# Kernel optimization log

Measured on AMD Instinct MI355X. Metric: run time of the kernel, lower is better.

## Reference

```python
import jax, jax.numpy as jnp
import numpy as np

WS = (7, 7)   # window size
SS = (3, 3)   # shift size
NH = 3        # num heads
EPS = 1e-5


def _rel_index():
    # relative position index [N, N], computed exactly as in WindowAttention.__init__
    coords = np.stack(np.meshgrid(np.arange(WS[0]), np.arange(WS[1]), indexing='ij'))  # [2,7,7]
    cf = coords.reshape(2, -1)                     # [2, N]
    rel = (cf[:, :, None] - cf[:, None, :]).transpose(1, 2, 0)  # [N, N, 2]
    rel[..., 0] += WS[0] - 1
    rel[..., 1] += WS[1] - 1
    idx = rel[..., 0] * (2 * WS[1] - 1) + rel[..., 1]
    return jnp.asarray(idx)


def _attn_mask(H, W):
    # standard Swin shifted-window mask: [nW, N, N] of {0, -100}
    img = np.zeros((H, W), dtype=np.float32)
    cnt = 0
    for hs in (slice(0, -WS[0]), slice(-WS[0], -SS[0]), slice(-SS[0], None)):
        for ws_ in (slice(0, -WS[1]), slice(-WS[1], -SS[1]), slice(-SS[1], None)):
            img[hs, ws_] = cnt
            cnt += 1
    mw = img.reshape(H // WS[0], WS[0], W // WS[1], WS[1]).transpose(0, 2, 1, 3)
    mw = mw.reshape(-1, WS[0] * WS[1])            # [nW, N]
    am = mw[:, None, :] - mw[:, :, None]
    am = np.where(am != 0, np.float32(-100.0), np.float32(0.0))
    return jnp.asarray(am)


def _ln(x, g, b):
    m = x.mean(-1, keepdims=True)
    v = ((x - m) ** 2).mean(-1, keepdims=True)
    return (x - m) * jax.lax.rsqrt(v + EPS) * g + b


def _forward(x, norm1_g, norm1_b, qkv_w, qkv_b, rel_table, proj_w, proj_b,
             norm2_g, norm2_b, mlp_w1, mlp_b1, mlp_w2, mlp_b2):
    B, C, H, W = x.shape
    N = WS[0] * WS[1]
    hd = C // NH
    scale = hd ** -0.5

    # norm1 over channels (token layout [B, HW, C])
    xt = x.reshape(B, C, H * W).transpose(0, 2, 1)
    xn = _ln(xt, norm1_g, norm1_b).transpose(0, 2, 1).reshape(B, C, H, W)

    # cyclic shift + window partition -> [B*nW, N, C]
    shifted = jnp.roll(xn, (-SS[0], -SS[1]), axis=(2, 3))
    nWh, nWw = H // WS[0], W // WS[1]
    xw = shifted.transpose(0, 2, 3, 1)  # [B, H, W, C]
    xwin = xw.reshape(B, nWh, WS[0], nWw, WS[1], C).transpose(0, 1, 3, 2, 4, 5)
    xwin = xwin.reshape(-1, N, C)

    # windowed attention with relative position bias + shift mask
    qkv = (xwin @ qkv_w.T + qkv_b).reshape(-1, N, 3, NH, hd).transpose(2, 0, 3, 1, 4)
    q, k, v = qkv[0] * scale, qkv[1], qkv[2]            # [B_, h, N, hd]
    attn = jnp.einsum('bhnd,bhmd->bhnm', q, k)          # [B_, h, N, N]
    bias = rel_table[_rel_index()]                       # [N, N, h]
    attn = attn + bias.transpose(2, 0, 1)[None]
    mask = _attn_mask(H, W)                              # [nW, N, N]
    nW = mask.shape[0]
    attn = attn.reshape(-1, nW, NH, N, N) + mask[None, :, None]
    attn = jax.nn.softmax(attn.reshape(-1, NH, N, N), axis=-1)
    out = jnp.einsum('bhnm,bhmd->bhnd', attn, v).transpose(0, 2, 1, 3).reshape(-1, N, C)
    out = out @ proj_w.T + proj_b

    # window reverse + reverse shift -> [B, C, H, W]
    xr = out.reshape(B, nWh, nWw, WS[0], WS[1], C).transpose(0, 1, 3, 2, 4, 5)
    xr = xr.reshape(B, H, W, C).transpose(0, 3, 1, 2)
    xr = jnp.roll(xr, (SS[0], SS[1]), axis=(2, 3))

    x = x + xr  # residual (drop_path = Identity)

    # MLP branch with pre-norm over channels
    xt = x.reshape(B, C, H * W).transpose(0, 2, 1)
    h = _ln(xt, norm2_g, norm2_b)
    h = jax.nn.gelu(h @ mlp_w1.T + mlp_b1, approximate=False)
    h = h @ mlp_w2.T + mlp_b2
    return x + h.transpose(0, 2, 1).reshape(B, C, H, W)


def setup_inputs() -> dict:
    key = jax.random.key(0)
    ks = jax.random.split(key, 8)
    B, C, H, W = 8, 96, 224, 224
    hid = 384
    s = 0.02
    return {
        'x': jax.random.normal(ks[0], (B, C, H, W), jnp.float32),
        'norm1_g': jnp.ones((C,), jnp.float32),
        'norm1_b': jnp.zeros((C,), jnp.float32),
        'qkv_w': jax.random.normal(ks[1], (3 * C, C), jnp.float32) * s,
        'qkv_b': jnp.zeros((3 * C,), jnp.float32),
        'rel_table': jax.random.normal(ks[2], (169, NH), jnp.float32) * s,
        'proj_w': jax.random.normal(ks[3], (C, C), jnp.float32) * s,
        'proj_b': jnp.zeros((C,), jnp.float32),
        'norm2_g': jnp.ones((C,), jnp.float32),
        'norm2_b': jnp.zeros((C,), jnp.float32),
        'mlp_w1': jax.random.normal(ks[4], (hid, C), jnp.float32) * s,
        'mlp_b1': jnp.zeros((hid,), jnp.float32),
        'mlp_w2': jax.random.normal(ks[5], (C, hid), jnp.float32) * s,
        'mlp_b2': jnp.zeros((C,), jnp.float32),
    }


def reference(x, norm1_g, norm1_b, qkv_w, qkv_b, rel_table, proj_w, proj_b,
              norm2_g, norm2_b, mlp_w1, mlp_b1, mlp_w2, mlp_b2):
    return _forward(x, norm1_g, norm1_b, qkv_w, qkv_b, rel_table, proj_w, proj_b,
                    norm2_g, norm2_b, mlp_w1, mlp_b1, mlp_w2, mlp_b2)
```

## Files before the change

kernel.cpp:

```cpp
#include <hip/hip_runtime.h>
#include <hip/hip_bf16.h>

typedef __attribute__((ext_vector_type(8))) short short8;
typedef __attribute__((ext_vector_type(4))) short s16x4;
typedef __attribute__((ext_vector_type(4))) float f32x4;

#define D_H   224
#define D_W   224
#define D_HW  50176
#define SCALE 0.17677669529663687f

#define WO_QKVW  0
#define WO_PROJW 27648
#define WO_W1    36864
#define WO_W2    73728
#define WO_TOT   110592

#define XT_SH 0
#define YT_SH 38535168
#define W_SH  77070336
#define WS_NEED ((size_t)(77070336 + 110592) * 2)

static __device__ __forceinline__ short f2s(float v) {
    union { __hip_bfloat16 b; short s; } u; u.b = __float2bfloat16(v); return u.s;
}
static __device__ __forceinline__ float s2f(short s) {
    union { short s; __hip_bfloat16 b; } u; u.s = s; return __bfloat162float(u.b);
}

#define MFMA(a, b, c) __builtin_amdgcn_mfma_f32_16x16x32_bf16((a), (b), (c), 0, 0, 0)

static __device__ __forceinline__ short8 normfrag(const short* p, const float* g,
                                                  const float* b, int c0, float m, float rs) {
    short8 r = *(const short8*)p;
    short8 o;
#pragma unroll
    for (int j = 0; j < 8; j++) o[j] = f2s((s2f(r[j]) - m) * rs * g[c0 + j] + b[c0 + j]);
    return o;
}

static __device__ __forceinline__ float erf_fast(float x) {
    float a = fabsf(x);
    float t = __builtin_amdgcn_rcpf(1.f + 0.3275911f * a);
    float p = t * (0.254829592f + t * (-0.284496736f + t * (1.421413741f +
              t * (-1.453152027f + t * 1.061405429f))));
    float y = 1.f - p * __expf(-a * a);
    return copysignf(y, x);
}

__global__ __launch_bounds__(256) void k_prep(
    const float* __restrict__ qkvw, const float* __restrict__ projw,
    const float* __restrict__ w1, const float* __restrict__ w2, short* __restrict__ ws)
{
    int i4 = blockIdx.x * 256 + threadIdx.x;
    const float* src; int off;
    if (i4 < 6912)        { src = qkvw;  off = 0; }
    else if (i4 < 9216)   { src = projw; off = 6912; }
    else if (i4 < 18432)  { src = w1;    off = 9216; }
    else                  { src = w2;    off = 18432; }
    f32x4 v = *(const f32x4*)&src[(i4 - off) * 4];
    s16x4 s;
#pragma unroll
    for (int j = 0; j < 4; j++) s[j] = f2s(v[j]);
    *(s16x4*)&ws[i4 * 4] = s;
}

__global__ __launch_bounds__(256) void k_t(const float* __restrict__ x, short* __restrict__ xt)
{
    __shared__ short tile[224][96];
    const int tid = threadIdx.x;
    const int bh = blockIdx.x;
    const int b = bh / 224, h = bh - b * 224;
    const int pbase = (b * 96) * D_HW + h * 224;

#pragma unroll
    for (int k = 0; k < 21; k++) {
        int idx = tid + k * 256;
        int w = idx % 224, u = idx / 224;
        int c0 = u * 4;
        s16x4 v;
        v[0] = f2s(x[pbase + (c0 + 0) * D_HW + w]);
        v[1] = f2s(x[pbase + (c0 + 1) * D_HW + w]);
        v[2] = f2s(x[pbase + (c0 + 2) * D_HW + w]);
        v[3] = f2s(x[pbase + (c0 + 3) * D_HW + w]);
        int slot = (u + w) % 24;
        *(s16x4*)&tile[w][slot * 4] = v;
    }
    __syncthreads();
    const int obase = ((b * 224 + h) * 224) * 96;
#pragma unroll
    for (int k = 0; k < 11; k++) {
        int idx = tid + k * 256;
        if (idx < 2688) {
            int w = idx / 12, s = idx - w * 12;
            int sl0 = (s * 2 + w) % 24, sl1 = (s * 2 + 1 + w) % 24;
            s16x4 a = *(const s16x4*)&tile[w][sl0 * 4];
            s16x4 c = *(const s16x4*)&tile[w][sl1 * 4];
            short8 o;
            o[0] = a[0]; o[1] = a[1]; o[2] = a[2]; o[3] = a[3];
            o[4] = c[0]; o[5] = c[1]; o[6] = c[2]; o[7] = c[3];
            *(short8*)&xt[obase + w * 96 + s * 8] = o;
        }
    }
}

__global__ __launch_bounds__(256, 3) void k_attn_t(
    const short* __restrict__ xt, const float* __restrict__ n1g, const float* __restrict__ n1b,
    const float* __restrict__ qkvb, const float* __restrict__ relt,
    const float* __restrict__ projb, const short* __restrict__ wsw, short* __restrict__ yt)
{
    __shared__ short qk[64][200];
    __shared__ __align__(16) short region[11520];
    short (*xs)[104] = (short(*)[104])region;
    short (*ps)[72]  = (short(*)[72])region;
    short (*vt)[72]  = (short(*)[72])(region + 4608);
    __shared__ int   cnt_s[64];
    __shared__ float mean_s[64], rstd_s[64];

    const int tid  = threadIdx.x;
    const int wave = tid >> 6, lane = tid & 63;
    const int l16  = lane & 15, q8 = (lane >> 4) * 8, q4 = (lane >> 4) * 4;
    const int t0   = wave * 16;

    const short* qkvw_bf  = wsw + WO_QKVW;
    const short* projw_bf = wsw + WO_PROJW;

    const int wi = blockIdx.x;
    const int b  = wi >> 10, nw = wi & 1023;
    const int wh = nw >> 5, ww = nw & 31;
    const bool edge = (wh == 31) || (ww == 31);

    if (tid < 64) {
        int t = (tid < 49) ? tid : 48;
        int r = t / 7, c = t - r * 7;
        int sh = wh * 7 + r, sw = ww * 7 + c;
        int rh = (sh < 217) ? 0 : ((sh < 221) ? 1 : 2);
        int rw = (sw < 217) ? 0 : ((sw < 221) ? 1 : 2);
        cnt_s[tid] = rh * 3 + rw;
    }
#pragma unroll
    for (int k = 0; k < 3; k++) {
        int idx = tid + k * 256;
        int t = idx / 12, s = idx - t * 12;
        short8 v = {0, 0, 0, 0, 0, 0, 0, 0};
        if (t < 49) {
            int r = t / 7, cc = t - r * 7;
            int hh = wh * 7 + r + 3;  if (hh >= D_H) hh -= D_H;
            int w2 = ww * 7 + cc + 3; if (w2 >= D_W) w2 -= D_W;
            v = *(const short8*)&xt[((b * 224 + hh) * 224 + w2) * 96 + s * 8];
        }
        *(short8*)&xs[t][s * 8] = v;
    }
    __syncthreads();

    {
        int t = tid >> 2, p = tid & 3;
        float s = 0.f, s2 = 0.f;
#pragma unroll
        for (int i = 0; i < 6; i++) {
            s16x4 v4 = *(const s16x4*)&xs[t][p * 24 + i * 4];
#pragma unroll
            for (int j = 0; j < 4; j++) { float v = s2f(v4[j]); s += v; s2 += v * v; }
        }
        s += __shfl_xor(s, 1); s2 += __shfl_xor(s2, 1);
        s += __shfl_xor(s, 2); s2 += __shfl_xor(s2, 2);
        if (p == 0) {
            float m = s * (1.f / 96.f);
            float var = s2 * (1.f / 96.f) - m * m;
            mean_s[t] = m; rstd_s[t] = rsqrtf(var + 1e-5f);
        }
    }

    const float m0 = mean_s[t0 + l16], rs0 = rstd_s[t0 + l16];
    short8 a0 = normfrag(&xs[t0 + l16][q8],      n1g, n1b, q8,      m0, rs0);
    short8 a1 = normfrag(&xs[t0 + l16][32 + q8], n1g, n1b, 32 + q8, m0, rs0);
    short8 a2 = normfrag(&xs[t0 + l16][64 + q8], n1g, n1b, 64 + q8, m0, rs0);

    short8 wA0, wA1, wA2, wB0, wB1, wB2;
    {
        const short* w = qkvw_bf + l16 * 96;
        wA0 = *(const short8*)&w[q8];
        wA1 = *(const short8*)&w[32 + q8];
        wA2 = *(const short8*)&w[64 + q8];
    }
    __syncthreads();

#pragma unroll
    for (int g = 0; g < 18; g++) {
        const int jc = g / 6, nt = g - jc * 6;
        const int jj = nt * 16 + l16;
        if (g < 17) {
            int g2 = g + 1, jc2 = g2 / 6, nt2 = g2 - jc2 * 6;
            const short* w = qkvw_bf + (jc2 * 96 + nt2 * 16 + l16) * 96;
            wB0 = *(const short8*)&w[q8];
            wB1 = *(const short8*)&w[32 + q8];
            wB2 = *(const short8*)&w[64 + q8];
        }
        f32x4 acc = {0.f, 0.f, 0.f, 0.f};
        acc = MFMA(a0, wA0, acc);
        acc = MFMA(a1, wA1, acc);
        acc = MFMA(a2, wA2, acc);
        float bias = qkvb[jc * 96 + jj];
        if (jc == 0) {
#pragma unroll
            for (int r = 0; r < 4; r++) qk[t0 + q4 + r][jj] = f2s((acc[r] + bias) * SCALE);
        } else if (jc == 1) {
#pragma unroll
            for (int r = 0; r < 4; r++) qk[t0 + q4 + r][96 + jj] = f2s(acc[r] + bias);
        } else {
            s16x4 v4;
#pragma unroll
            for (int r = 0; r < 4; r++) v4[r] = f2s(acc[r] + bias);
            *(s16x4*)&vt[jj][t0 + q4] = v4;
        }
        wA0 = wB0; wA1 = wB1; wA2 = wB2;
    }

    float biasv[4][4][3];
#pragma unroll
    for (int nt = 0; nt < 4; nt++) {
        int m  = nt * 16 + l16;
        int mm = (m < 49) ? m : 48;
        int r2 = mm / 7, c2 = mm - r2 * 7;
        int cm = cnt_s[m];
#pragma unroll
        for (int r = 0; r < 4; r++) {
            int n  = t0 + q4 + r;
            int nn = (n < 49) ? n : 48;
            int r1 = nn / 7, c1 = nn - r1 * 7;
            int ri = ((r1 - r2 + 6) * 13 + (c1 - c2 + 6)) * 3;
            float mk = (edge && (cnt_s[n] != cm)) ? -100.f : 0.f;
            biasv[nt][r][0] = relt[ri + 0] + mk;
            biasv[nt][r][1] = relt[ri + 1] + mk;
            biasv[nt][r][2] = relt[ri + 2] + mk;
        }
    }
    const bool inval3 = (l16 != 0);

    __syncthreads();

#pragma unroll
    for (int h = 0; h < 3; h++) {
        short8 aq = *(const short8*)&qk[t0 + l16][h * 32 + q8];
        f32x4 sv[4];
#pragma unroll
        for (int nt = 0; nt < 4; nt++) {
            f32x4 z = {0.f, 0.f, 0.f, 0.f};
            sv[nt] = MFMA(aq, *(const short8*)&qk[nt * 16 + l16][96 + h * 32 + q8], z);
        }
        float mx[4] = {-1e30f, -1e30f, -1e30f, -1e30f};
#pragma unroll
        for (int nt = 0; nt < 4; nt++) {
#pragma unroll
            for (int r = 0; r < 4; r++) {
                float v = sv[nt][r] + biasv[nt][r][h];
                if (nt == 3 && inval3) v = -1e30f;
                sv[nt][r] = v;
                mx[r] = fmaxf(mx[r], v);
            }
        }
#pragma unroll
        for (int d = 1; d < 16; d <<= 1) {
#pragma unroll
            for (int r = 0; r < 4; r++) mx[r] = fmaxf(mx[r], __shfl_xor(mx[r], d));
        }
        float sm[4] = {0.f, 0.f, 0.f, 0.f};
#pragma unroll
        for (int nt = 0; nt < 4; nt++) {
#pragma unroll
            for (int r = 0; r < 4; r++) {
                float e = (nt == 3 && inval3) ? 0.f : __expf(sv[nt][r] - mx[r]);
                sv[nt][r] = e;
                sm[r] += e;
            }
        }
#pragma unroll
        for (int d = 1; d < 16; d <<= 1) {
#pragma unroll
            for (int r = 0; r < 4; r++) sm[r] += __shfl_xor(sm[r], d);
        }
        float inv[4];
#pragma unroll
        for (int r = 0; r < 4; r++) inv[r] = __builtin_amdgcn_rcpf(sm[r]);
#pragma unroll
        for (int nt = 0; nt < 4; nt++) {
#pragma unroll
            for (int r = 0; r < 4; r++)
                ps[t0 + q4 + r][nt * 16 + l16] = f2s(sv[nt][r] * inv[r]);
        }
        short8 p0 = *(const short8*)&ps[t0 + l16][q8];
        short8 p1 = *(const short8*)&ps[t0 + l16][32 + q8];
#pragma unroll
        for (int nt = 0; nt < 2; nt++) {
            f32x4 acc = {0.f, 0.f, 0.f, 0.f};
            acc = MFMA(p0, *(const short8*)&vt[h * 32 + nt * 16 + l16][q8],      acc);
            acc = MFMA(p1, *(const short8*)&vt[h * 32 + nt * 16 + l16][32 + q8], acc);
            int d = nt * 16 + l16;
#pragma unroll
            for (int r = 0; r < 4; r++) {
                int t = t0 + q4 + r;
                if (t < 49) qk[t][h * 32 + d] = f2s(acc[r]);
            }
        }
    }

    {
        const short* w = projw_bf + l16 * 96;
        wA0 = *(const short8*)&w[q8];
        wA1 = *(const short8*)&w[32 + q8];
        wA2 = *(const short8*)&w[64 + q8];
    }
    short8 o0 = *(const short8*)&qk[t0 + l16][q8];
    short8 o1 = *(const short8*)&qk[t0 + l16][32 + q8];
    short8 o2 = *(const short8*)&qk[t0 + l16][64 + q8];
#pragma unroll
    for (int nt = 0; nt < 6; nt++) {
        int i = nt * 16 + l16;
        if (nt < 5) {
            const short* w = projw_bf + ((nt + 1) * 16 + l16) * 96;
            wB0 = *(const short8*)&w[q8];
            wB1 = *(const short8*)&w[32 + q8];
            wB2 = *(const short8*)&w[64 + q8];
        }
        f32x4 acc = {0.f, 0.f, 0.f, 0.f};
        acc = MFMA(o0, wA0, acc);
        acc = MFMA(o1, wA1, acc);
        acc = MFMA(o2, wA2, acc);
        float pb = projb[i];
#pragma unroll
        for (int r = 0; r < 4; r++) {
            int t = t0 + q4 + r;
            if (t < 49) qk[t][i] = f2s(acc[r] + pb);
        }
        wA0 = wB0; wA1 = wB1; wA2 = wB2;
    }
    __syncthreads();
#pragma unroll
    for (int k = 0; k < 3; k++) {
        int idx = tid + k * 256;
        if (idx < 588) {
            int t = idx / 12, s = idx - t * 12;
            int r = t / 7, cc = t - r * 7;
            int hh = wh * 7 + r + 3;  if (hh >= D_H) hh -= D_H;
            int w2 = ww * 7 + cc + 3; if (w2 >= D_W) w2 -= D_W;
            *(short8*)&yt[((b * 224 + hh) * 224 + w2) * 96 + s * 8] =
                *(const short8*)&qk[t][s * 8];
        }
    }
}

#define XCOL(row, c) ((((((c) >> 3) ^ (((row) >> 2) & 7)) << 3)) | ((c) & 7))

__global__ __launch_bounds__(256, 3) void k_mlp_t(
    const float* __restrict__ x, const short* __restrict__ ytk, float* __restrict__ y,
    const float* __restrict__ n2g, const float* __restrict__ n2b,
    const float* __restrict__ b1, const float* __restrict__ b2, const short* __restrict__ wsw)
{
    __shared__ __align__(16) short xs[64][128];
    __shared__ __align__(16) short wb[96][104];
    __shared__ __align__(16) short hb[64][104];
    __shared__ float mean_s[64], rstd_s[64];

    const int tid  = threadIdx.x;
    const int wave = tid >> 6, lane = tid & 63;
    const int l16  = lane & 15, q8 = (lane >> 4) * 8, q4 = (lane >> 4) * 4;
    const int t0   = wave * 16;

    const short* w1_bf = wsw + WO_W1;
    const short* w2_bf = wsw + WO_W2;

    const int T0 = blockIdx.x * 64;
    const int b  = T0 / D_HW;
    const int p0 = T0 - b * D_HW;
    const int base = (b * 96) * D_HW + p0;

#pragma unroll
    for (int k = 0; k < 3; k++) {
        int idx = tid + k * 256;
        int t = idx / 12, s = idx - t * 12;
        *(short8*)&xs[t][(s ^ ((t >> 2) & 7)) << 3] =
            *(const short8*)&ytk[(T0 + t) * 96 + s * 8];
    }
    __syncthreads();

    float yv[6][4];
#pragma unroll
    for (int k = 0; k < 6; k++) {
        int idx = tid + k * 256;
        int c = idx >> 4, q = idx & 15;
        f32x4 xv = *(const f32x4*)&x[base + c * D_HW + q * 4];
        int ch = ((c >> 3) ^ (q & 7)) * 8 + (c & 7);
#pragma unroll
        for (int j = 0; j < 4; j++) {
            float v = xv[j] + s2f(xs[q * 4 + j][ch]);
            yv[k][j] = v;
            xs[q * 4 + j][ch] = f2s(v);
        }
    }
    __syncthreads();

    {
        int t = tid >> 2, p = tid & 3;
        float s = 0.f, s2 = 0.f;
#pragma unroll
        for (int i = 0; i < 6; i++) {
            int c = p * 24 + i * 4;
            s16x4 v4 = *(const s16x4*)&xs[t][XCOL(t, c)];
#pragma unroll
            for (int j = 0; j < 4; j++) { float v = s2f(v4[j]); s += v; s2 += v * v; }
        }
        s += __shfl_xor(s, 1); s2 += __shfl_xor(s2, 1);
        s += __shfl_xor(s, 2); s2 += __shfl_xor(s2, 2);
        if (p == 0) {
            float m = s * (1.f / 96.f);
            float var = s2 * (1.f / 96.f) - m * m;
            mean_s[t] = m; rstd_s[t] = rsqrtf(var + 1e-5f);
        }
    }

    short8 xa[3];
    {
        int t = t0 + l16;
        float m = mean_s[t], rs = rstd_s[t];
        int key = (t >> 2) & 7;
#pragma unroll
        for (int kk = 0; kk < 3; kk++) {
            int ch = kk * 4 + (lane >> 4);
            xa[kk] = normfrag(&xs[t][(ch ^ key) << 3], n2g, n2b, ch * 8, m, rs);
        }
    }

    f32x4 c2[6];
#pragma unroll
    for (int nt = 0; nt < 6; nt++) c2[nt] = (f32x4){0.f, 0.f, 0.f, 0.f};

    short8 pf[5];
#pragma unroll
    for (int k = 0; k < 5; k++) {
        int idx = tid + k * 256; if (idx > 1151) idx = 1151;
        pf[k] = *(const short8*)&w1_bf[idx * 8];
    }
#pragma unroll
    for (int jc = 0; jc < 4; jc++) {
        if (jc > 0) __syncthreads();
#pragma unroll
        for (int k = 0; k < 5; k++) {
            int idx = tid + k * 256;
            if (idx < 1152) { int j = idx / 12, s = idx - j * 12; *(short8*)&wb[j][s * 8] = pf[k]; }
        }
        __syncthreads();
#pragma unroll
        for (int k = 0; k < 5; k++) {
            int idx = tid + k * 256; if (idx > 1151) idx = 1151;
            int o = idx / 12, s = idx - o * 12;
            pf[k] = *(const short8*)&w2_bf[o * 384 + jc * 96 + s * 8];
        }
#pragma unroll
        for (int nt = 0; nt < 6; nt++) {
            int jj = nt * 16 + l16;
            f32x4 acc = {0.f, 0.f, 0.f, 0.f};
            acc = MFMA(xa[0], *(const short8*)&wb[jj][q8],      acc);
            acc = MFMA(xa[1], *(const short8*)&wb[jj][32 + q8], acc);
            acc = MFMA(xa[2], *(const short8*)&wb[jj][64 + q8], acc);
            float bb = b1[jc * 96 + jj];
#pragma unroll
            for (int r = 0; r < 4; r++) {
                float v = acc[r] + bb;
                float g = 0.5f * v * (1.f + erf_fast(v * 0.7071067811865475f));
                hb[t0 + q4 + r][jj] = f2s(g);
            }
        }
        __syncthreads();
#pragma unroll
        for (int k = 0; k < 5; k++) {
            int idx = tid + k * 256;
            if (idx < 1152) { int j = idx / 12, s = idx - j * 12; *(short8*)&wb[j][s * 8] = pf[k]; }
        }
        __syncthreads();
        if (jc < 3) {
#pragma unroll
            for (int k = 0; k < 5; k++) {
                int idx = tid + k * 256; if (idx > 1151) idx = 1151;
                pf[k] = *(const short8*)&w1_bf[(jc + 1) * 9216 + idx * 8];
            }
        }
        {
            short8 h0 = *(const short8*)&hb[t0 + l16][q8];
            short8 h1 = *(const short8*)&hb[t0 + l16][32 + q8];
            short8 h2 = *(const short8*)&hb[t0 + l16][64 + q8];
#pragma unroll
            for (int nt = 0; nt < 6; nt++) {
                int jj = nt * 16 + l16;
                c2[nt] = MFMA(h0, *(const short8*)&wb[jj][q8],      c2[nt]);
                c2[nt] = MFMA(h1, *(const short8*)&wb[jj][32 + q8], c2[nt]);
                c2[nt] = MFMA(h2, *(const short8*)&wb[jj][64 + q8], c2[nt]);
            }
        }
    }

#pragma unroll
    for (int nt = 0; nt < 6; nt++) {
        int i = nt * 16 + l16;
        float bo = b2[i];
#pragma unroll
        for (int r = 0; r < 4; r++) {
            int t = t0 + q4 + r;
            xs[t][XCOL(t, i)] = f2s(bo + c2[nt][r]);
        }
    }
    __syncthreads();
#pragma unroll
    for (int k = 0; k < 6; k++) {
        int idx = tid + k * 256;
        int c = idx >> 4, q = idx & 15;
        int ch = ((c >> 3) ^ (q & 7)) * 8 + (c & 7);
        f32x4 o;
#pragma unroll
        for (int j = 0; j < 4; j++) o[j] = yv[k][j] + s2f(xs[q * 4 + j][ch]);
        *(f32x4*)&y[base + c * D_HW + q * 4] = o;
    }
}

__global__ __launch_bounds__(256, 3) void k_attn_f(
    const float* __restrict__ x, const float* __restrict__ n1g, const float* __restrict__ n1b,
    const float* __restrict__ qkvb, const float* __restrict__ relt,
    const float* __restrict__ projb, const short* __restrict__ wsw, float* __restrict__ y)
{
    __shared__ short qk[64][200];
    __shared__ short vt[96][72];
    __shared__ __align__(16) short xs[64][104];
    short (*ps)[72] = (short(*)[72])xs;
    __shared__ int   cnt_s[64];
    __shared__ float mean_s[64], rstd_s[64];

    const int tid  = threadIdx.x;
    const int wave = tid >> 6, lane = tid & 63;
    const int l16  = lane & 15, q8 = (lane >> 4) * 8, q4 = (lane >> 4) * 4;
    const int t0   = wave * 16;

    const short* qkvw_bf  = wsw + WO_QKVW;
    const short* projw_bf = wsw + WO_PROJW;

    const int wi = blockIdx.x;
    const int b  = wi >> 10, nw = wi & 1023;
    const int wh = nw >> 5, ww = nw & 31;
    const bool edge = (wh == 31) || (ww == 31);

    if (tid < 64) {
        int t = (tid < 49) ? tid : 48;
        int r = t / 7, c = t - r * 7;
        int sh = wh * 7 + r, sw = ww * 7 + c;
        int rh = (sh < 217) ? 0 : ((sh < 221) ? 1 : 2);
        int rw = (sw < 217) ? 0 : ((sw < 221) ? 1 : 2);
        cnt_s[tid] = rh * 3 + rw;
    }
    {
        int t = lane;
        int r = t / 7, cc = t - r * 7;
        int hh = wh * 7 + r + 3;  if (hh >= D_H) hh -= D_H;
        int w2 = ww * 7 + cc + 3; if (w2 >= D_W) w2 -= D_W;
        int off0 = (b * 96) * D_HW + hh * D_W + w2;
#pragma unroll
        for (int n = 0; n < 6; n++) {
            int c0 = wave * 24 + n * 4;
            s16x4 v4 = {0, 0, 0, 0};
            if (t < 49) {
                v4[0] = f2s(x[off0 + (c0 + 0) * D_HW]);
                v4[1] = f2s(x[off0 + (c0 + 1) * D_HW]);
                v4[2] = f2s(x[off0 + (c0 + 2) * D_HW]);
                v4[3] = f2s(x[off0 + (c0 + 3) * D_HW]);
            }
            *(s16x4*)&xs[t][c0] = v4;
        }
    }
    __syncthreads();
    {
        int t = tid >> 2, p = tid & 3;
        float s = 0.f, s2 = 0.f;
#pragma unroll
        for (int i = 0; i < 6; i++) {
            s16x4 v4 = *(const s16x4*)&xs[t][p * 24 + i * 4];
#pragma unroll
            for (int j = 0; j < 4; j++) { float v = s2f(v4[j]); s += v; s2 += v * v; }
        }
        s += __shfl_xor(s, 1); s2 += __shfl_xor(s2, 1);
        s += __shfl_xor(s, 2); s2 += __shfl_xor(s2, 2);
        if (p == 0) {
            float m = s * (1.f / 96.f);
            float var = s2 * (1.f / 96.f) - m * m;
            mean_s[t] = m; rstd_s[t] = rsqrtf(var + 1e-5f);
        }
    }
    __syncthreads();

    const float m0 = mean_s[t0 + l16], rs0 = rstd_s[t0 + l16];
    short8 a0 = normfrag(&xs[t0 + l16][q8],      n1g, n1b, q8,      m0, rs0);
    short8 a1 = normfrag(&xs[t0 + l16][32 + q8], n1g, n1b, 32 + q8, m0, rs0);
    short8 a2 = normfrag(&xs[t0 + l16][64 + q8], n1g, n1b, 64 + q8, m0, rs0);

#pragma unroll
    for (int jc = 0; jc < 3; jc++) {
#pragma unroll
        for (int nt = 0; nt < 6; nt++) {
            int jj = nt * 16 + l16;
            const short* wr = qkvw_bf + (jc * 96 + jj) * 96;
            f32x4 acc = {0.f, 0.f, 0.f, 0.f};
            acc = MFMA(a0, *(const short8*)&wr[q8],      acc);
            acc = MFMA(a1, *(const short8*)&wr[32 + q8], acc);
            acc = MFMA(a2, *(const short8*)&wr[64 + q8], acc);
            float bias = qkvb[jc * 96 + jj];
            if (jc == 0) {
#pragma unroll
                for (int r = 0; r < 4; r++) qk[t0 + q4 + r][jj] = f2s((acc[r] + bias) * SCALE);
            } else if (jc == 1) {
#pragma unroll
                for (int r = 0; r < 4; r++) qk[t0 + q4 + r][96 + jj] = f2s(acc[r] + bias);
            } else {
                s16x4 v4;
#pragma unroll
                for (int r = 0; r < 4; r++) v4[r] = f2s(acc[r] + bias);
                *(s16x4*)&vt[jj][t0 + q4] = v4;
            }
        }
    }

    float biasv[4][4][3];
#pragma unroll
    for (int nt = 0; nt < 4; nt++) {
        int m  = nt * 16 + l16;
        int mm = (m < 49) ? m : 48;
        int r2 = mm / 7, c2 = mm - r2 * 7;
        int cm = cnt_s[m];
#pragma unroll
        for (int r = 0; r < 4; r++) {
            int n  = t0 + q4 + r;
            int nn = (n < 49) ? n : 48;
            int r1 = nn / 7, c1 = nn - r1 * 7;
            int ri = ((r1 - r2 + 6) * 13 + (c1 - c2 + 6)) * 3;
            float mk = (edge && (cnt_s[n] != cm)) ? -100.f : 0.f;
            biasv[nt][r][0] = relt[ri + 0] + mk;
            biasv[nt][r][1] = relt[ri + 1] + mk;
            biasv[nt][r][2] = relt[ri + 2] + mk;
        }
    }
    const bool inval3 = (l16 != 0);

#pragma unroll
    for (int h = 0; h < 3; h++) {
        __syncthreads();
        short8 aq = *(const short8*)&qk[t0 + l16][h * 32 + q8];
        f32x4 sv[4];
#pragma unroll
        for (int nt = 0; nt < 4; nt++) {
            f32x4 z = {0.f, 0.f, 0.f, 0.f};
            sv[nt] = MFMA(aq, *(const short8*)&qk[nt * 16 + l16][96 + h * 32 + q8], z);
        }
        float mx[4] = {-1e30f, -1e30f, -1e30f, -1e30f};
#pragma unroll
        for (int nt = 0; nt < 4; nt++) {
#pragma unroll
            for (int r = 0; r < 4; r++) {
                float v = sv[nt][r] + biasv[nt][r][h];
                if (nt == 3 && inval3) v = -1e30f;
                sv[nt][r] = v;
                mx[r] = fmaxf(mx[r], v);
            }
        }
#pragma unroll
        for (int d = 1; d < 16; d <<= 1) {
#pragma unroll
            for (int r = 0; r < 4; r++) mx[r] = fmaxf(mx[r], __shfl_xor(mx[r], d));
        }
        float sm[4] = {0.f, 0.f, 0.f, 0.f};
#pragma unroll
        for (int nt = 0; nt < 4; nt++) {
#pragma unroll
            for (int r = 0; r < 4; r++) {
                float e = (nt == 3 && inval3) ? 0.f : __expf(sv[nt][r] - mx[r]);
                sv[nt][r] = e;
                sm[r] += e;
            }
        }
#pragma unroll
        for (int d = 1; d < 16; d <<= 1) {
#pragma unroll
            for (int r = 0; r < 4; r++) sm[r] += __shfl_xor(sm[r], d);
        }
        float inv[4];
#pragma unroll
        for (int r = 0; r < 4; r++) inv[r] = 1.f / sm[r];
#pragma unroll
        for (int nt = 0; nt < 4; nt++) {
#pragma unroll
            for (int r = 0; r < 4; r++)
                ps[t0 + q4 + r][nt * 16 + l16] = f2s(sv[nt][r] * inv[r]);
        }
        __syncthreads();
        short8 p0 = *(const short8*)&ps[t0 + l16][q8];
        short8 p1 = *(const short8*)&ps[t0 + l16][32 + q8];
#pragma unroll
        for (int nt = 0; nt < 2; nt++) {
            f32x4 acc = {0.f, 0.f, 0.f, 0.f};
            acc = MFMA(p0, *(const short8*)&vt[h * 32 + nt * 16 + l16][q8],      acc);
            acc = MFMA(p1, *(const short8*)&vt[h * 32 + nt * 16 + l16][32 + q8], acc);
            int d = nt * 16 + l16;
#pragma unroll
            for (int r = 0; r < 4; r++) {
                int t = t0 + q4 + r;
                if (t < 49) qk[t][h * 32 + d] = f2s(acc[r]);
            }
        }
    }

    __syncthreads();
    short8 o0 = *(const short8*)&qk[t0 + l16][q8];
    short8 o1 = *(const short8*)&qk[t0 + l16][32 + q8];
    short8 o2 = *(const short8*)&qk[t0 + l16][64 + q8];
    int  po[4];
    bool tv[4];
#pragma unroll
    for (int r = 0; r < 4; r++) {
        int t = t0 + q4 + r;
        tv[r] = (t < 49);
        int tt = tv[r] ? t : 0;
        int rr = tt / 7, cc = tt - rr * 7;
        int hh = wh * 7 + rr + 3;  if (hh >= D_H) hh -= D_H;
        int w2 = ww * 7 + cc + 3;  if (w2 >= D_W) w2 -= D_W;
        po[r] = (b * 96) * D_HW + hh * D_W + w2;
    }
#pragma unroll
    for (int nt = 0; nt < 6; nt++) {
        int i = nt * 16 + l16;
        const short* wr = projw_bf + i * 96;
        f32x4 acc = {0.f, 0.f, 0.f, 0.f};
        acc = MFMA(o0, *(const short8*)&wr[q8],      acc);
        acc = MFMA(o1, *(const short8*)&wr[32 + q8], acc);
        acc = MFMA(o2, *(const short8*)&wr[64 + q8], acc);
        float pb = projb[i];
#pragma unroll
        for (int r = 0; r < 4; r++) {
            if (tv[r]) {
                int off = po[r] + i * D_HW;
                y[off] = x[off] + acc[r] + pb;
            }
        }
    }
}

__global__ __launch_bounds__(256, 3) void k_mlp_f(
    float* __restrict__ y, const float* __restrict__ n2g, const float* __restrict__ n2b,
    const float* __restrict__ b1, const float* __restrict__ b2, const short* __restrict__ wsw)
{
    __shared__ short xs[128][104];
    __shared__ short hb[128][104];
    __shared__ float mean_s[128], rstd_s[128];

    const int tid  = threadIdx.x;
    const int wave = tid >> 6, lane = tid & 63;
    const int l16  = lane & 15, q8 = (lane >> 4) * 8, q4 = (lane >> 4) * 4;
    const int t0   = wave * 32;

    const short* w1_bf = wsw + WO_W1;
    const short* w2_bf = wsw + WO_W2;

    const int T0 = blockIdx.x * 128;
    const int b  = T0 / D_HW;
    const int p0 = T0 - b * D_HW;
    const int base = (b * 96) * D_HW + p0;

    for (int idx = tid; idx < 96 * 32; idx += 256) {
        int c = idx >> 5, q = idx & 31;
        f32x4 v4 = *(const f32x4*)&y[base + c * D_HW + q * 4];
        xs[q * 4 + 0][c] = f2s(v4[0]);
        xs[q * 4 + 1][c] = f2s(v4[1]);
        xs[q * 4 + 2][c] = f2s(v4[2]);
        xs[q * 4 + 3][c] = f2s(v4[3]);
    }
    __syncthreads();
    {
        int t = tid >> 1, p = tid & 1;
        float s = 0.f, s2 = 0.f;
#pragma unroll
        for (int i = 0; i < 12; i++) {
            s16x4 v4 = *(const s16x4*)&xs[t][p * 48 + i * 4];
#pragma unroll
            for (int j = 0; j < 4; j++) { float v = s2f(v4[j]); s += v; s2 += v * v; }
        }
        s += __shfl_xor(s, 1); s2 += __shfl_xor(s2, 1);
        float m = s * (1.f / 96.f);
        float var = s2 * (1.f / 96.f) - m * m;
        mean_s[t] = m; rstd_s[t] = rsqrtf(var + 1e-5f);
    }
    __syncthreads();

    short8 xa[2][3];
#pragma unroll
    for (int s = 0; s < 2; s++) {
        float m = mean_s[t0 + s * 16 + l16], rs = rstd_s[t0 + s * 16 + l16];
#pragma unroll
        for (int kk = 0; kk < 3; kk++)
            xa[s][kk] = normfrag(&xs[t0 + s * 16 + l16][kk * 32 + q8], n2g, n2b,
                                 kk * 32 + q8, m, rs);
    }

    f32x4 c2[2][6];
#pragma unroll
    for (int s = 0; s < 2; s++)
#pragma unroll
        for (int nt = 0; nt < 6; nt++) c2[s][nt] = (f32x4){0.f, 0.f, 0.f, 0.f};

    for (int jc = 0; jc < 4; jc++) {
#pragma unroll
        for (int s = 0; s < 2; s++) {
#pragma unroll
            for (int nt = 0; nt < 6; nt++) {
                int jj = nt * 16 + l16;
                const short* wr = w1_bf + (jc * 96 + jj) * 96;
                f32x4 acc = {0.f, 0.f, 0.f, 0.f};
                acc = MFMA(xa[s][0], *(const short8*)&wr[q8],      acc);
                acc = MFMA(xa[s][1], *(const short8*)&wr[32 + q8], acc);
                acc = MFMA(xa[s][2], *(const short8*)&wr[64 + q8], acc);
                float bb = b1[jc * 96 + jj];
#pragma unroll
                for (int r = 0; r < 4; r++) {
                    float v = acc[r] + bb;
                    float g = 0.5f * v * (1.f + erf_fast(v * 0.7071067811865475f));
                    hb[t0 + s * 16 + q4 + r][jj] = f2s(g);
                }
            }
        }
        __syncthreads();
#pragma unroll
        for (int s = 0; s < 2; s++) {
            short8 h0 = *(const short8*)&hb[t0 + s * 16 + l16][q8];
            short8 h1 = *(const short8*)&hb[t0 + s * 16 + l16][32 + q8];
            short8 h2 = *(const short8*)&hb[t0 + s * 16 + l16][64 + q8];
#pragma unroll
            for (int nt = 0; nt < 6; nt++) {
                const short* wr = w2_bf + (nt * 16 + l16) * 384 + jc * 96;
                c2[s][nt] = MFMA(h0, *(const short8*)&wr[q8],      c2[s][nt]);
                c2[s][nt] = MFMA(h1, *(const short8*)&wr[32 + q8], c2[s][nt]);
                c2[s][nt] = MFMA(h2, *(const short8*)&wr[64 + q8], c2[s][nt]);
            }
        }
        __syncthreads();
    }

#pragma unroll
    for (int s = 0; s < 2; s++)
#pragma unroll
        for (int nt = 0; nt < 6; nt++) {
            int i = nt * 16 + l16;
            float bo = b2[i];
#pragma unroll
            for (int r = 0; r < 4; r++)
                xs[t0 + s * 16 + q4 + r][i] = f2s(bo + c2[s][nt][r]);
        }
    __syncthreads();
    for (int idx = tid; idx < 96 * 32; idx += 256) {
        int c = idx >> 5, q = idx & 31;
        int off = base + c * D_HW + q * 4;
        f32x4 v4 = *(const f32x4*)&y[off];
        v4[0] += s2f(xs[q * 4 + 0][c]);
        v4[1] += s2f(xs[q * 4 + 1][c]);
        v4[2] += s2f(xs[q * 4 + 2][c]);
        v4[3] += s2f(xs[q * 4 + 3][c]);
        *(f32x4*)&y[off] = v4;
    }
}

extern "C" void kernel_launch(void* const* d_in, const int* in_sizes, int n_in,
                              void* d_out, int out_size, void* d_ws, size_t ws_size,
                              hipStream_t stream) {
    const float* x    = (const float*)d_in[0];
    const float* n1g  = (const float*)d_in[1];
    const float* n1b  = (const float*)d_in[2];
    const float* qkvw = (const float*)d_in[3];
    const float* qkvb = (const float*)d_in[4];
    const float* relt = (const float*)d_in[5];
    const float* projw= (const float*)d_in[6];
    const float* projb= (const float*)d_in[7];
    const float* n2g  = (const float*)d_in[8];
    const float* n2b  = (const float*)d_in[9];
    const float* w1   = (const float*)d_in[10];
    const float* b1   = (const float*)d_in[11];
    const float* w2   = (const float*)d_in[12];
    const float* b2   = (const float*)d_in[13];
    float* y  = (float*)d_out;
    short* ws = (short*)d_ws;

    if (ws_size >= WS_NEED) {
        short* xt  = ws + XT_SH;
        short* ytk = ws + YT_SH;
        short* wbf = ws + W_SH;
        k_prep<<<108, 256, 0, stream>>>(qkvw, projw, w1, w2, wbf);
        k_t<<<1792, 256, 0, stream>>>(x, xt);
        k_attn_t<<<8192, 256, 0, stream>>>(xt, n1g, n1b, qkvb, relt, projb, wbf, ytk);
        k_mlp_t<<<6272, 256, 0, stream>>>(x, ytk, y, n2g, n2b, b1, b2, wbf);
    } else {
        k_prep<<<108, 256, 0, stream>>>(qkvw, projw, w1, w2, ws);
        k_attn_f<<<8192, 256, 0, stream>>>(x, n1g, n1b, qkvb, relt, projb, ws, y);
        k_mlp_f<<<3136, 256, 0, stream>>>(y, n2g, n2b, b1, b2, ws);
    }
}
```

Before: 638.6 us.

## Load MLP weights directly into registers and vectorize transpose loads

The MLP kernel no longer stages W1/W2 tiles through shared memory with block barriers. Each wave now loads its MFMA B-fragments straight from global (L2-resident) bf16 weights into registers, prefetching one tile ahead, and occupancy is raised to 4 blocks. Separately, the input transpose kernel switches to float4 row loads into a channel-major XOR-swizzled tile and gathers columns on readout. The aim is to remove LDS traffic and barriers, at the cost of more global/L2 reads per wave and scalar LDS reads in the transpose.

```diff
diff --git a/kernel.cpp b/kernel.cpp
--- a/kernel.cpp
+++ b/kernel.cpp
@@ -67,7 +67,7 @@
 
 __global__ __launch_bounds__(256) void k_t(const float* __restrict__ x, short* __restrict__ xt)
 {
-    __shared__ short tile[224][96];
+    __shared__ short tile[96][232];
     const int tid = threadIdx.x;
     const int bh = blockIdx.x;
     const int b = bh / 224, h = bh - b * 224;
@@ -76,15 +76,13 @@
 #pragma unroll
     for (int k = 0; k < 21; k++) {
         int idx = tid + k * 256;
-        int w = idx % 224, u = idx / 224;
-        int c0 = u * 4;
-        s16x4 v;
-        v[0] = f2s(x[pbase + (c0 + 0) * D_HW + w]);
-        v[1] = f2s(x[pbase + (c0 + 1) * D_HW + w]);
-        v[2] = f2s(x[pbase + (c0 + 2) * D_HW + w]);
-        v[3] = f2s(x[pbase + (c0 + 3) * D_HW + w]);
-        int slot = (u + w) % 24;
-        *(s16x4*)&tile[w][slot * 4] = v;
+        int c = idx / 56, w4 = idx - c * 56;
+        f32x4 v = *(const f32x4*)&x[pbase + c * D_HW + w4 * 4];
+        s16x4 s;
+#pragma unroll
+        for (int j = 0; j < 4; j++) s[j] = f2s(v[j]);
+        int col = (w4 * 4) ^ ((((c >> 3) ^ c) & 7) << 2);
+        *(s16x4*)&tile[c][col] = s;
     }
     __syncthreads();
     const int obase = ((b * 224 + h) * 224) * 96;
@@ -93,12 +91,12 @@
         int idx = tid + k * 256;
         if (idx < 2688) {
             int w = idx / 12, s = idx - w * 12;
-            int sl0 = (s * 2 + w) % 24, sl1 = (s * 2 + 1 + w) % 24;
-            s16x4 a = *(const s16x4*)&tile[w][sl0 * 4];
-            s16x4 c = *(const s16x4*)&tile[w][sl1 * 4];
             short8 o;
-            o[0] = a[0]; o[1] = a[1]; o[2] = a[2]; o[3] = a[3];
-            o[4] = c[0]; o[5] = c[1]; o[6] = c[2]; o[7] = c[3];
+#pragma unroll
+            for (int j = 0; j < 8; j++) {
+                int c = s * 8 + j;
+                o[j] = tile[c][w ^ ((((c >> 3) ^ c) & 7) << 2)];
+            }
             *(short8*)&xt[obase + w * 96 + s * 8] = o;
         }
     }
@@ -351,13 +349,12 @@
 
 #define XCOL(row, c) ((((((c) >> 3) ^ (((row) >> 2) & 7)) << 3)) | ((c) & 7))
 
-__global__ __launch_bounds__(256, 3) void k_mlp_t(
+__global__ __launch_bounds__(256, 4) void k_mlp_t(
     const float* __restrict__ x, const short* __restrict__ ytk, float* __restrict__ y,
     const float* __restrict__ n2g, const float* __restrict__ n2b,
     const float* __restrict__ b1, const float* __restrict__ b2, const short* __restrict__ wsw)
 {
     __shared__ __align__(16) short xs[64][128];
-    __shared__ __align__(16) short wb[96][104];
     __shared__ __align__(16) short hb[64][104];
     __shared__ float mean_s[64], rstd_s[64];
 
@@ -434,34 +431,33 @@
 #pragma unroll
     for (int nt = 0; nt < 6; nt++) c2[nt] = (f32x4){0.f, 0.f, 0.f, 0.f};
 
-    short8 pf[5];
-#pragma unroll
-    for (int k = 0; k < 5; k++) {
-        int idx = tid + k * 256; if (idx > 1151) idx = 1151;
-        pf[k] = *(const short8*)&w1_bf[idx * 8];
+    short8 wA0, wA1, wA2, wB0, wB1, wB2;
+    {
+        const short* w = w1_bf + l16 * 96;
+        wA0 = *(const short8*)&w[q8];
+        wA1 = *(const short8*)&w[32 + q8];
+        wA2 = *(const short8*)&w[64 + q8];
     }
 #pragma unroll
     for (int jc = 0; jc < 4; jc++) {
-        if (jc > 0) __syncthreads();
-#pragma unroll
-        for (int k = 0; k < 5; k++) {
-            int idx = tid + k * 256;
-            if (idx < 1152) { int j = idx / 12, s = idx - j * 12; *(short8*)&wb[j][s * 8] = pf[k]; }
-        }
-        __syncthreads();
-#pragma unroll
-        for (int k = 0; k < 5; k++) {
-            int idx = tid + k * 256; if (idx > 1151) idx = 1151;
-            int o = idx / 12, s = idx - o * 12;
-            pf[k] = *(const short8*)&w2_bf[o * 384 + jc * 96 + s * 8];
-        }
 #pragma unroll
         for (int nt = 0; nt < 6; nt++) {
             int jj = nt * 16 + l16;
+            if (nt < 5) {
+                const short* w = w1_bf + (jc * 96 + (nt + 1) * 16 + l16) * 96;
+                wB0 = *(const short8*)&w[q8];
+                wB1 = *(const short8*)&w[32 + q8];
+                wB2 = *(const short8*)&w[64 + q8];
+            } else {
+                const short* w = w2_bf + l16 * 384 + jc * 96;
+                wB0 = *(const short8*)&w[q8];
+                wB1 = *(const short8*)&w[32 + q8];
+                wB2 = *(const short8*)&w[64 + q8];
+            }
             f32x4 acc = {0.f, 0.f, 0.f, 0.f};
-            acc = MFMA(xa[0], *(const short8*)&wb[jj][q8],      acc);
-            acc = MFMA(xa[1], *(const short8*)&wb[jj][32 + q8], acc);
-            acc = MFMA(xa[2], *(const short8*)&wb[jj][64 + q8], acc);
+            acc = MFMA(xa[0], wA0, acc);
+            acc = MFMA(xa[1], wA1, acc);
+            acc = MFMA(xa[2], wA2, acc);
             float bb = b1[jc * 96 + jj];
 #pragma unroll
             for (int r = 0; r < 4; r++) {
@@ -469,32 +465,28 @@
                 float g = 0.5f * v * (1.f + erf_fast(v * 0.7071067811865475f));
                 hb[t0 + q4 + r][jj] = f2s(g);
             }
-        }
-        __syncthreads();
-#pragma unroll
-        for (int k = 0; k < 5; k++) {
-            int idx = tid + k * 256;
-            if (idx < 1152) { int j = idx / 12, s = idx - j * 12; *(short8*)&wb[j][s * 8] = pf[k]; }
-        }
-        __syncthreads();
-        if (jc < 3) {
-#pragma unroll
-            for (int k = 0; k < 5; k++) {
-                int idx = tid + k * 256; if (idx > 1151) idx = 1151;
-                pf[k] = *(const short8*)&w1_bf[(jc + 1) * 9216 + idx * 8];
-            }
-        }
-        {
-            short8 h0 = *(const short8*)&hb[t0 + l16][q8];
-            short8 h1 = *(const short8*)&hb[t0 + l16][32 + q8];
-            short8 h2 = *(const short8*)&hb[t0 + l16][64 + q8];
-#pragma unroll
-            for (int nt = 0; nt < 6; nt++) {
-                int jj = nt * 16 + l16;
-                c2[nt] = MFMA(h0, *(const short8*)&wb[jj][q8],      c2[nt]);
-                c2[nt] = MFMA(h1, *(const short8*)&wb[jj][32 + q8], c2[nt]);
-                c2[nt] = MFMA(h2, *(const short8*)&wb[jj][64 + q8], c2[nt]);
-            }
+            wA0 = wB0; wA1 = wB1; wA2 = wB2;
+        }
+        short8 h0 = *(const short8*)&hb[t0 + l16][q8];
+        short8 h1 = *(const short8*)&hb[t0 + l16][32 + q8];
+        short8 h2 = *(const short8*)&hb[t0 + l16][64 + q8];
+#pragma unroll
+        for (int nt = 0; nt < 6; nt++) {
+            if (nt < 5) {
+                const short* w = w2_bf + ((nt + 1) * 16 + l16) * 384 + jc * 96;
+                wB0 = *(const short8*)&w[q8];
+                wB1 = *(const short8*)&w[32 + q8];
+                wB2 = *(const short8*)&w[64 + q8];
+            } else if (jc < 3) {
+                const short* w = w1_bf + ((jc + 1) * 96 + l16) * 96;
+                wB0 = *(const short8*)&w[q8];
+                wB1 = *(const short8*)&w[32 + q8];
+                wB2 = *(const short8*)&w[64 + q8];
+            }
+            c2[nt] = MFMA(h0, wA0, c2[nt]);
+            c2[nt] = MFMA(h1, wA1, c2[nt]);
+            c2[nt] = MFMA(h2, wA2, c2[nt]);
+            wA0 = wB0; wA1 = wB1; wA2 = wB2;
         }
     }
 
```

Result: slower. 807.7 us (+26.5%).
